# Performance work log

Measured on AMD Instinct MI355X. Metric: run time of the kernel, lower is better.

The kernel has to match this reference:

```python
import jax, jax.numpy as jnp
import numpy as np

DIM = 768
HEADS = 12
HEAD_DIM = DIM // HEADS
SCALE = HEAD_DIM ** -0.5
ALPHA = 0.1


def setup_inputs() -> dict:
    key = jax.random.key(0)
    ks = jax.random.split(key, 6)
    B, N, C = 16, 577, DIM
    x = jax.random.normal(ks[0], (B, N, C), dtype=jnp.float32)
    attn_weight = jax.random.uniform(ks[1], (B, N - 1), dtype=jnp.float32)
    w_qkv = jax.random.normal(ks[2], (C, 3 * C), dtype=jnp.float32) * (C ** -0.5)
    b_qkv = jnp.zeros((3 * C,), dtype=jnp.float32)
    w_proj = jax.random.normal(ks[3], (C, C), dtype=jnp.float32) * (C ** -0.5)
    b_proj = jnp.zeros((C,), dtype=jnp.float32)
    return {"x": x, "attn_weight": attn_weight, "w_qkv": w_qkv, "b_qkv": b_qkv,
            "w_proj": w_proj, "b_proj": b_proj}


def reference(x, attn_weight, w_qkv, b_qkv, w_proj, b_proj):
    B, N, C = x.shape
    H, D = HEADS, HEAD_DIM
    qkv = (x @ w_qkv + b_qkv).reshape(B, N, 3, H, D)
    qkv = jnp.transpose(qkv, (2, 0, 3, 1, 4))  # [3, B, H, N, D]
    q, k, v = qkv[0], qkv[1], qkv[2]
    attn = jnp.einsum('bhnd,bhmd->bhnm', q, k) * SCALE  # [B,H,N,N]
    patch_attn = attn[:, :, 0, 1:]  # pre-softmax CLS->patch scores
    # reweight CLS row (excluding CLS->CLS) before softmax
    w = attn_weight[:, None, None, :]  # [B,1,1,N-1]
    cls_row = attn[:, :, 0:1, 1:] * (w * ALPHA + (1.0 - ALPHA))
    attn = attn.at[:, :, 0:1, 1:].set(cls_row)
    attn = jax.nn.softmax(attn, axis=-1)
    out = jnp.einsum('bhnm,bhmd->bhnd', attn, v)
    out = jnp.transpose(out, (0, 2, 1, 3)).reshape(B, N, C)
    out = out @ w_proj + b_proj
    return out, patch_attn
```

## Files before the change

kernel.cpp:

```cpp
#include <hip/hip_runtime.h>
#include <hip/hip_bf16.h>
#include <math.h>

#define B_    16
#define N_    577
#define C_    768
#define H_    12
#define D_    64
#define M_    (B_ * N_)
#define MP_   9344
#define QKVN  2304
#define NP_   640
#define SCALE 0.125f
#define ALPHA 0.1f
#define OUT0  (B_ * N_ * C_)

#define NB_CONV 7008
#define NB_T1   1728
#define NB_T2   576

typedef __attribute__((ext_vector_type(8))) short short8;
typedef __attribute__((ext_vector_type(4))) float f32x4;
typedef __hip_bfloat16 bf16;

__device__ __forceinline__ float exp2fast(float x) {
    return __builtin_amdgcn_exp2f(x);
}

__device__ __forceinline__ void load16(const void* g, void* l) {
    __builtin_amdgcn_global_load_lds(
        (const __attribute__((address_space(1))) unsigned int*)g,
        (__attribute__((address_space(3))) unsigned int*)l, 16, 0, 0);
}

__device__ __forceinline__ f32x4 mfma16(short8 a, short8 b, f32x4 c) {
    return __builtin_amdgcn_mfma_f32_16x16x32_bf16(a, b, c, 0, 0, 0);
}

#define FENCE() asm volatile("" ::: "memory")
#define BARRIER() do { FENCE(); __builtin_amdgcn_s_barrier(); FENCE(); } while (0)

__global__ __launch_bounds__(256) void prep(const float* __restrict__ x,
                                            bf16* __restrict__ xb,
                                            const float* __restrict__ wq,
                                            bf16* __restrict__ wqT,
                                            const float* __restrict__ wp,
                                            bf16* __restrict__ wpT) {
    __shared__ float tile[32][33];
    const int bid = blockIdx.x;
    if (bid < NB_CONV) {
        int idx = bid * 256 + threadIdx.x;
        int m = idx / 192;
        bf16 tmp[4];
        if (m < M_) {
            float4 f = ((const float4*)x)[idx];
            tmp[0] = __float2bfloat16(f.x);
            tmp[1] = __float2bfloat16(f.y);
            tmp[2] = __float2bfloat16(f.z);
            tmp[3] = __float2bfloat16(f.w);
        } else {
            tmp[0] = tmp[1] = tmp[2] = tmp[3] = __float2bfloat16(0.f);
        }
        ((ushort4*)xb)[idx] = *(ushort4*)tmp;
        return;
    }
    const float* src; bf16* dst; int C, R, bx, by;
    if (bid < NB_CONV + NB_T1) {
        int r = bid - NB_CONV;
        bx = r % 72; by = r / 72; src = wq; dst = wqT; R = 768; C = QKVN;
    } else {
        int r = bid - NB_CONV - NB_T1;
        bx = r % 24; by = r / 24; src = wp; dst = wpT; R = 768; C = 768;
    }
    int cb = bx * 32, rb = by * 32;
    int tx = threadIdx.x & 31, ty = threadIdx.x >> 5;
    #pragma unroll
    for (int i = 0; i < 32; i += 8)
        tile[ty + i][tx] = src[(size_t)(rb + ty + i) * C + cb + tx];
    __syncthreads();
    #pragma unroll
    for (int i = 0; i < 32; i += 8)
        dst[(size_t)(cb + ty + i) * R + rb + tx] = __float2bfloat16(tile[tx][ty + i]);
}

__global__ __launch_bounds__(256, 4) void gemm128(const bf16* __restrict__ A,
                                                  const bf16* __restrict__ BT,
                                                  const float* __restrict__ bias,
                                                  bf16* __restrict__ q,
                                                  bf16* __restrict__ kk,
                                                  bf16* __restrict__ vt,
                                                  float* __restrict__ out,
                                                  int mode, int nby) {
    __shared__ __align__(16) char smem[35840];

    const int nwg = gridDim.x;
    const int orig = blockIdx.x;
    const int xcd = orig & 7, ii = orig >> 3;
    const int qq = nwg >> 3, rr = nwg & 7;
    const int wg = (xcd < rr ? xcd * (qq + 1) : rr * (qq + 1) + (xcd - rr) * qq) + ii;
    const int mb = wg / nby;
    const int nb = wg - mb * nby;
    const int m0 = mb * 128, n0 = nb * 128;
    const int t = threadIdx.x, lane = t & 63, w = t >> 6;
    const int wr = w >> 1, wc = w & 1;
    const int r16 = lane & 15, quad = lane >> 4;

    f32x4 acc[4][4];
    #pragma unroll
    for (int i = 0; i < 4; i++)
        #pragma unroll
        for (int j = 0; j < 4; j++) acc[i][j] = (f32x4)(0.f);

    const int lrow = lane >> 3;
    const int clog = ((lane & 7) ^ lrow) << 4;
    const char* gA = (const char*)A  + (size_t)(m0 + w * 32 + lrow) * 1536 + clog;
    const char* gB = (const char*)BT + (size_t)(n0 + w * 32 + lrow) * 1536 + clog;

    auto stage = [&](int k2) {
        const int kc = k2 * 128;
        #pragma unroll
        for (int i = 0; i < 4; i++) {
            char* dA = (char*)smem + w * 4096 + i * 1024;
            load16(gA + (size_t)i * 12288 + kc, dA);
            load16(gB + (size_t)i * 12288 + kc, dA + 16384);
        }
    };

    stage(0);
    asm volatile("s_waitcnt vmcnt(0)" ::: "memory");
    BARRIER();

    const int sw = r16 & 7;
    const int g0 = (quad ^ sw) << 4;
    const int g1 = ((quad ^ 4) ^ sw) << 4;

    #pragma unroll 1
    for (int k = 0; k < 12; k++) {
        const char* Ap = (const char*)smem + (wr * 64 + r16) * 128;
        const char* Bp = (const char*)smem + 16384 + (wc * 64 + r16) * 128;

        short8 a[4], b[4];
        #pragma unroll
        for (int mi = 0; mi < 4; mi++) a[mi] = *(const short8*)(Ap + mi * 2048 + g0);
        #pragma unroll
        for (int nj = 0; nj < 4; nj++) b[nj] = *(const short8*)(Bp + nj * 2048 + g0);
        __builtin_amdgcn_s_setprio(1);
        #pragma unroll
        for (int mi = 0; mi < 4; mi++)
            #pragma unroll
            for (int nj = 0; nj < 4; nj++)
                acc[mi][nj] = mfma16(a[mi], b[nj], acc[mi][nj]);
        __builtin_amdgcn_s_setprio(0);

        #pragma unroll
        for (int mi = 0; mi < 4; mi++) a[mi] = *(const short8*)(Ap + mi * 2048 + g1);
        #pragma unroll
        for (int nj = 0; nj < 4; nj++) b[nj] = *(const short8*)(Bp + nj * 2048 + g1);
        __builtin_amdgcn_s_setprio(1);
        #pragma unroll
        for (int mi = 0; mi < 4; mi++)
            #pragma unroll
            for (int nj = 0; nj < 4; nj++)
                acc[mi][nj] = mfma16(a[mi], b[nj], acc[mi][nj]);
        __builtin_amdgcn_s_setprio(0);

        BARRIER();
        if (k < 11) {
            stage(k + 1);
            asm volatile("s_waitcnt vmcnt(0)" ::: "memory");
            BARRIER();
        }
    }

    float bs[4];
    #pragma unroll
    for (int nj = 0; nj < 4; nj++) bs[nj] = bias[n0 + wc * 64 + nj * 16 + r16];

    if (mode == 1) {
        #pragma unroll
        for (int mi = 0; mi < 4; mi++) {
            #pragma unroll
            for (int nj = 0; nj < 4; nj++) {
                #pragma unroll
                for (int r = 0; r < 4; r++) {
                    int m = m0 + wr * 64 + mi * 16 + quad * 4 + r;
                    if (m >= M_) continue;
                    int cc = n0 + wc * 64 + nj * 16 + r16;
                    out[(size_t)m * 768 + cc] = acc[mi][nj][r] + bs[nj];
                }
            }
        }
        return;
    }

    bf16* Tt = (bf16*)smem;
    #pragma unroll
    for (int mi = 0; mi < 4; mi++) {
        #pragma unroll
        for (int nj = 0; nj < 4; nj++) {
            bf16 pk[4];
            #pragma unroll
            for (int r = 0; r < 4; r++)
                pk[r] = __float2bfloat16(acc[mi][nj][r] + bs[nj]);
            int ccl = wc * 64 + nj * 16 + r16;
            int ml4 = wr * 64 + mi * 16 + quad * 4;
            *(uint2*)&Tt[ccl * 140 + ml4] = *(const uint2*)pk;
        }
    }
    __syncthreads();

    const int part = nb / 6;
    if (part < 2) {
        int nl = t & 127, half = t >> 7;
        int m = m0 + nl;
        if (m < M_) {
            int b = m / N_, n = m - b * N_;
            int h = (nb % 6) * 2 + half;
            bf16* dst = (part == 0 ? q : kk) + ((size_t)(b * H_ + h) * N_ + n) * 64;
            #pragma unroll
            for (int d8 = 0; d8 < 8; d8++) {
                bf16 tv[8];
                #pragma unroll
                for (int dd = 0; dd < 8; dd++)
                    tv[dd] = Tt[(half * 64 + d8 * 8 + dd) * 140 + nl];
                *(uint4*)(dst + d8 * 8) = *(const uint4*)tv;
            }
        }
    } else {
        int dr = t >> 1, seg = t & 1;
        int rem = (nb % 6) * 128 + dr;
        int h = rem >> 6, d = rem & 63;
        int mb2 = m0 + seg * 64;
        int b = mb2 / N_;
        int n = mb2 - b * N_;
        const bf16* src = Tt + dr * 140 + seg * 64;
        int i = 0;
        while (i < 64 && mb2 + i < M_) {
            if (n == N_) { b++; n = 0; }
            bf16* drow = vt + ((size_t)(b * H_ + h) * 64 + d) * NP_;
            if ((n & 7) == 0 && n + 8 <= N_ && i + 8 <= 64 && mb2 + i + 8 <= M_) {
                bf16 tv[8];
                #pragma unroll
                for (int dd = 0; dd < 8; dd++) tv[dd] = src[i + dd];
                *(uint4*)(drow + n) = *(const uint4*)tv;
                i += 8; n += 8;
            } else {
                drow[n] = src[i]; i++; n++;
            }
        }
    }
}

__global__ __launch_bounds__(256) void attn_mfma(const bf16* __restrict__ q,
                                                 const bf16* __restrict__ k,
                                                 const bf16* __restrict__ vt,
                                                 const float* __restrict__ aw,
                                                 bf16* __restrict__ ao,
                                                 float* __restrict__ patch) {
    __shared__ bf16 Kb[2][4096];
    __shared__ bf16 Vb[2][4096];
    __shared__ bf16 Pb[4][2048];
    const int orig = blockIdx.x;
    const int wg = (orig & 7) * 120 + (orig >> 3);
    const int bh = wg / 5, qt = wg - bh * 5;
    const int b = bh / H_, h = bh - b * H_;
    const int t = threadIdx.x, lane = t & 63, w = t >> 6;
    const int r16 = lane & 15, quad = lane >> 4;
    const float SC2 = SCALE * 1.44269504f;

    const bf16* kbp = k + (size_t)bh * N_ * 64;
    const bf16* vbp = vt + (size_t)bh * 64 * NP_;

    short8 qa0[2], qa1[2];
    #pragma unroll
    for (int mi = 0; mi < 2; mi++) {
        int qrow = qt * 128 + w * 32 + mi * 16 + r16;
        int qrc = (qrow < N_) ? qrow : (N_ - 1);
        const bf16* qp = q + ((size_t)bh * N_ + qrc) * 64 + quad * 8;
        qa0[mi] = *(const short8*)(qp);
        qa1[mi] = *(const short8*)(qp + 32);
    }

    f32x4 Oacc[2][4];
    #pragma unroll
    for (int mi = 0; mi < 2; mi++)
        #pragma unroll
        for (int d0 = 0; d0 < 4; d0++) Oacc[mi][d0] = (f32x4)(0.f);
    float lrow[2][4];
    #pragma unroll
    for (int mi = 0; mi < 2; mi++)
        #pragma unroll
        for (int rr = 0; rr < 4; rr++) lrow[mi][rr] = 0.f;

    const bool clsrow = (qt == 0) && (w == 0) && (quad == 0);

    auto stage = [&](int kt, int buf) {
        #pragma unroll
        for (int is = 0; is < 2; is++) {
            int base = is * 256 + w * 64;
            int slot = base + lane;
            int row = slot >> 3, pos = slot & 7;
            int c = pos ^ (row & 7);
            int jg = kt * 64 + row; if (jg > N_ - 1) jg = N_ - 1;
            load16(kbp + (size_t)jg * 64 + c * 8, &Kb[buf][base * 8]);
        }
        #pragma unroll
        for (int is = 0; is < 2; is++) {
            int base = is * 256 + w * 64;
            int slot = base + lane;
            int row = slot >> 3, pos = slot & 7;
            int c = pos ^ (row & 7);
            load16(vbp + (size_t)row * NP_ + kt * 64 + c * 8, &Vb[buf][base * 8]);
        }
    };

    stage(0, 0);
    __syncthreads();

    for (int kt = 0; kt < 10; kt++) {
        const int cur = kt & 1;
        if (kt < 9) stage(kt + 1, cur ^ 1);

        f32x4 S[2][4];
        #pragma unroll
        for (int j0 = 0; j0 < 4; j0++) {
            int row = j0 * 16 + r16;
            const bf16* kpl = &Kb[cur][row * 64];
            short8 kf0 = *(const short8*)(kpl + ((quad ^ (row & 7)) << 3));
            short8 kf1 = *(const short8*)(kpl + (((quad ^ 4) ^ (row & 7)) << 3));
            #pragma unroll
            for (int mi = 0; mi < 2; mi++) {
                f32x4 sa = (f32x4)(0.f);
                sa = mfma16(qa0[mi], kf0, sa);
                sa = mfma16(qa1[mi], kf1, sa);
                S[mi][j0] = sa;
            }
        }

        if (kt < 9) {
            #pragma unroll
            for (int mi = 0; mi < 2; mi++) {
                #pragma unroll
                for (int j0 = 0; j0 < 4; j0++) {
                    float wfac = 1.f;
                    if (mi == 0 && clsrow) {
                        int c = kt * 64 + j0 * 16 + r16;
                        if (c >= 1) {
                            patch[(size_t)bh * (N_ - 1) + (c - 1)] = S[0][j0][0] * SCALE;
                            wfac = aw[b * (N_ - 1) + (c - 1)] * ALPHA + (1.f - ALPHA);
                        }
                    }
                    #pragma unroll
                    for (int rr = 0; rr < 4; rr++) {
                        float v = S[mi][j0][rr] * SC2;
                        if (rr == 0) v *= wfac;
                        float p = exp2fast(v);
                        S[mi][j0][rr] = p;
                        lrow[mi][rr] += p;
                    }
                }
            }
        } else {
            #pragma unroll
            for (int mi = 0; mi < 2; mi++) {
                #pragma unroll
                for (int j0 = 0; j0 < 4; j0++) {
                    int c = kt * 64 + j0 * 16 + r16;
                    bool valid = (c < N_);
                    float wfac = 1.f;
                    if (mi == 0 && clsrow && valid) {
                        patch[(size_t)bh * (N_ - 1) + (c - 1)] = S[0][j0][0] * SCALE;
                        wfac = aw[b * (N_ - 1) + (c - 1)] * ALPHA + (1.f - ALPHA);
                    }
                    #pragma unroll
                    for (int rr = 0; rr < 4; rr++) {
                        float v = S[mi][j0][rr] * SC2;
                        if (rr == 0) v *= wfac;
                        float p = valid ? exp2fast(v) : 0.f;
                        S[mi][j0][rr] = p;
                        lrow[mi][rr] += p;
                    }
                }
            }
        }

        bf16* pw = &Pb[w][0];
        #pragma unroll
        for (int mi = 0; mi < 2; mi++) {
            #pragma unroll
            for (int j0 = 0; j0 < 4; j0++) {
                int cg = j0 * 2 + (r16 >> 3);
                #pragma unroll
                for (int rr = 0; rr < 4; rr++) {
                    int rp = mi * 16 + quad * 4 + rr;
                    pw[rp * 64 + ((cg ^ (rp & 7)) << 3) + (r16 & 7)] =
                        __float2bfloat16(S[mi][j0][rr]);
                }
            }
        }
        short8 pa0[2], pa1[2];
        #pragma unroll
        for (int mi = 0; mi < 2; mi++) {
            int rp = mi * 16 + r16;
            const bf16* pr = pw + rp * 64;
            pa0[mi] = *(const short8*)(pr + ((quad ^ (rp & 7)) << 3));
            pa1[mi] = *(const short8*)(pr + (((quad ^ 4) ^ (rp & 7)) << 3));
        }

        #pragma unroll
        for (int d0 = 0; d0 < 4; d0++) {
            int row = d0 * 16 + r16;
            const bf16* vpl = &Vb[cur][row * 64];
            short8 vf0 = *(const short8*)(vpl + ((quad ^ (row & 7)) << 3));
            short8 vf1 = *(const short8*)(vpl + (((quad ^ 4) ^ (row & 7)) << 3));
            #pragma unroll
            for (int mi = 0; mi < 2; mi++) {
                Oacc[mi][d0] = mfma16(pa0[mi], vf0, Oacc[mi][d0]);
                Oacc[mi][d0] = mfma16(pa1[mi], vf1, Oacc[mi][d0]);
            }
        }
        __syncthreads();
    }

    #pragma unroll
    for (int mi = 0; mi < 2; mi++) {
        #pragma unroll
        for (int rr = 0; rr < 4; rr++) {
            float l = lrow[mi][rr];
            l += __shfl_xor(l, 1);
            l += __shfl_xor(l, 2);
            l += __shfl_xor(l, 4);
            l += __shfl_xor(l, 8);
            int n = qt * 128 + w * 32 + mi * 16 + quad * 4 + rr;
            if (n >= N_) continue;
            float inv = 1.f / l;
            #pragma unroll
            for (int d0 = 0; d0 < 4; d0++) {
                ao[((size_t)(b * N_ + n) * H_ + h) * 64 + d0 * 16 + r16] =
                    __float2bfloat16(Oacc[mi][d0][rr] * inv);
            }
        }
    }
}

extern "C" void kernel_launch(void* const* d_in, const int* in_sizes, int n_in,
                              void* d_out, int out_size, void* d_ws, size_t ws_size,
                              hipStream_t stream) {
    const float* x      = (const float*)d_in[0];
    const float* aw     = (const float*)d_in[1];
    const float* w_qkv  = (const float*)d_in[2];
    const float* b_qkv  = (const float*)d_in[3];
    const float* w_proj = (const float*)d_in[4];
    const float* b_proj = (const float*)d_in[5];
    float* out = (float*)d_out;

    char* ws = (char*)d_ws;
    bf16* xbf    = (bf16*)(ws);
    bf16* wqkvT  = (bf16*)(ws + 14352384);
    bf16* wprojT = (bf16*)(ws + 17891328);
    bf16* qv     = (bf16*)(ws + 19070976);
    bf16* kv     = (bf16*)(ws + 33251328);
    bf16* vt     = (bf16*)(ws + 47431680);
    bf16* ao     = xbf;

    prep<<<NB_CONV + NB_T1 + NB_T2, 256, 0, stream>>>(x, xbf, w_qkv, wqkvT, w_proj, wprojT);

    gemm128<<<73 * 18, 256, 0, stream>>>(
        xbf, wqkvT, b_qkv, qv, kv, vt, nullptr, 0, 18);

    attn_mfma<<<H_ * B_ * 5, 256, 0, stream>>>(qv, kv, vt, aw, ao, out + OUT0);

    gemm128<<<73 * 6, 256, 0, stream>>>(
        ao, wprojT, b_proj, nullptr, nullptr, nullptr, out, 1, 6);
}
```

Measured before the change: 208.5 us.

## Double-buffer A tile in LDS and load B fragments directly from global

The GEMM now double-buffers the A tile in shared memory, issuing the next stage's loads before the current MFMAs so global latency overlaps compute, and drops one barrier per k-step. B fragments are read straight from global memory into registers instead of being staged through LDS, which frees LDS and removes LDS reads for B. Launch bounds occupancy hint drops from 4 to 3 to give more registers. The risk is that uncoalesced per-lane global B loads and lower occupancy may hurt, and the B loads sit just before the MFMAs with little latency hiding.

```diff
diff --git a/kernel.cpp b/kernel.cpp
--- a/kernel.cpp
+++ b/kernel.cpp
@@ -83,7 +83,7 @@
         dst[(size_t)(cb + ty + i) * R + rb + tx] = __float2bfloat16(tile[tx][ty + i]);
 }
 
-__global__ __launch_bounds__(256, 4) void gemm128(const bf16* __restrict__ A,
+__global__ __launch_bounds__(256, 3) void gemm128(const bf16* __restrict__ A,
                                                   const bf16* __restrict__ BT,
                                                   const float* __restrict__ bias,
                                                   bf16* __restrict__ q,
@@ -113,18 +113,17 @@
 
     const int lrow = lane >> 3;
     const int clog = ((lane & 7) ^ lrow) << 4;
-    const char* gA = (const char*)A  + (size_t)(m0 + w * 32 + lrow) * 1536 + clog;
-    const char* gB = (const char*)BT + (size_t)(n0 + w * 32 + lrow) * 1536 + clog;
+    const char* gA = (const char*)A + (size_t)(m0 + w * 32 + lrow) * 1536 + clog;
 
     auto stage = [&](int k2) {
         const int kc = k2 * 128;
-        #pragma unroll
-        for (int i = 0; i < 4; i++) {
-            char* dA = (char*)smem + w * 4096 + i * 1024;
-            load16(gA + (size_t)i * 12288 + kc, dA);
-            load16(gB + (size_t)i * 12288 + kc, dA + 16384);
-        }
+        char* dA = (char*)smem + (k2 & 1) * 16384 + w * 4096;
+        #pragma unroll
+        for (int i = 0; i < 4; i++)
+            load16(gA + (size_t)i * 12288 + kc, dA + i * 1024);
     };
+
+    const bf16* pb = BT + (size_t)(n0 + wc * 64 + r16) * 768 + quad * 8;
 
     stage(0);
     asm volatile("s_waitcnt vmcnt(0)" ::: "memory");
@@ -136,40 +135,38 @@
 
     #pragma unroll 1
     for (int k = 0; k < 12; k++) {
-        const char* Ap = (const char*)smem + (wr * 64 + r16) * 128;
-        const char* Bp = (const char*)smem + 16384 + (wc * 64 + r16) * 128;
-
-        short8 a[4], b[4];
+        const char* Ap = (const char*)smem + (k & 1) * 16384 + (wr * 64 + r16) * 128;
+        short8 a[4], b0[4], b1[4];
+
+        #pragma unroll
+        for (int nj = 0; nj < 4; nj++) {
+            b0[nj] = *(const short8*)(pb + nj * 12288 + k * 64);
+            b1[nj] = *(const short8*)(pb + nj * 12288 + k * 64 + 32);
+        }
+        if (k < 11) stage(k + 1);
+
         #pragma unroll
         for (int mi = 0; mi < 4; mi++) a[mi] = *(const short8*)(Ap + mi * 2048 + g0);
-        #pragma unroll
-        for (int nj = 0; nj < 4; nj++) b[nj] = *(const short8*)(Bp + nj * 2048 + g0);
         __builtin_amdgcn_s_setprio(1);
         #pragma unroll
         for (int mi = 0; mi < 4; mi++)
             #pragma unroll
             for (int nj = 0; nj < 4; nj++)
-                acc[mi][nj] = mfma16(a[mi], b[nj], acc[mi][nj]);
+                acc[mi][nj] = mfma16(a[mi], b0[nj], acc[mi][nj]);
         __builtin_amdgcn_s_setprio(0);
 
         #pragma unroll
         for (int mi = 0; mi < 4; mi++) a[mi] = *(const short8*)(Ap + mi * 2048 + g1);
-        #pragma unroll
-        for (int nj = 0; nj < 4; nj++) b[nj] = *(const short8*)(Bp + nj * 2048 + g1);
         __builtin_amdgcn_s_setprio(1);
         #pragma unroll
         for (int mi = 0; mi < 4; mi++)
             #pragma unroll
             for (int nj = 0; nj < 4; nj++)
-                acc[mi][nj] = mfma16(a[mi], b[nj], acc[mi][nj]);
+                acc[mi][nj] = mfma16(a[mi], b1[nj], acc[mi][nj]);
         __builtin_amdgcn_s_setprio(0);
 
+        if (k < 11) { asm volatile("s_waitcnt vmcnt(0)" ::: "memory"); }
         BARRIER();
-        if (k < 11) {
-            stage(k + 1);
-            asm volatile("s_waitcnt vmcnt(0)" ::: "memory");
-            BARRIER();
-        }
     }
 
     float bs[4];
@@ -194,6 +191,7 @@
     }
 
     bf16* Tt = (bf16*)smem;
+    __syncthreads();
     #pragma unroll
     for (int mi = 0; mi < 4; mi++) {
         #pragma unroll
```

Result: slower. 261.5 us (+25.4%).

## Widen GEMM tiles to 128x256 with 512-thread workgroups

Applied to the files above, without the earlier changes.

The bf16 MFMA GEMM now computes a 128x256 output tile per workgroup using 8 waves (2x4) instead of a 128x128 tile with 4 waves. The A tile is shared across twice as many output columns, which cuts global and LDS traffic for A. The epilogue is split into two phases that reuse the same LDS transpose buffer for q/k/vt scatter. The price is fewer workgroups (657 and 219), which may underfill the GPU, plus higher LDS use per block.

```diff
diff --git a/kernel.cpp b/kernel.cpp
--- a/kernel.cpp
+++ b/kernel.cpp
@@ -83,15 +83,15 @@
         dst[(size_t)(cb + ty + i) * R + rb + tx] = __float2bfloat16(tile[tx][ty + i]);
 }
 
-__global__ __launch_bounds__(256, 4) void gemm128(const bf16* __restrict__ A,
-                                                  const bf16* __restrict__ BT,
-                                                  const float* __restrict__ bias,
-                                                  bf16* __restrict__ q,
-                                                  bf16* __restrict__ kk,
-                                                  bf16* __restrict__ vt,
-                                                  float* __restrict__ out,
-                                                  int mode, int nby) {
-    __shared__ __align__(16) char smem[35840];
+__global__ __launch_bounds__(512, 6) void gemmn(const bf16* __restrict__ A,
+                                                const bf16* __restrict__ BT,
+                                                const float* __restrict__ bias,
+                                                bf16* __restrict__ q,
+                                                bf16* __restrict__ kk,
+                                                bf16* __restrict__ vt,
+                                                float* __restrict__ out,
+                                                int mode, int nby) {
+    __shared__ __align__(16) char smem[49152];
 
     const int nwg = gridDim.x;
     const int orig = blockIdx.x;
@@ -100,9 +100,9 @@
     const int wg = (xcd < rr ? xcd * (qq + 1) : rr * (qq + 1) + (xcd - rr) * qq) + ii;
     const int mb = wg / nby;
     const int nb = wg - mb * nby;
-    const int m0 = mb * 128, n0 = nb * 128;
+    const int m0 = mb * 128, n0 = nb * 256;
     const int t = threadIdx.x, lane = t & 63, w = t >> 6;
-    const int wr = w >> 1, wc = w & 1;
+    const int wr = w >> 2, wc = w & 3;
     const int r16 = lane & 15, quad = lane >> 4;
 
     f32x4 acc[4][4];
@@ -113,16 +113,17 @@
 
     const int lrow = lane >> 3;
     const int clog = ((lane & 7) ^ lrow) << 4;
-    const char* gA = (const char*)A  + (size_t)(m0 + w * 32 + lrow) * 1536 + clog;
-    const char* gB = (const char*)BT + (size_t)(n0 + w * 32 + lrow) * 1536 + clog;
+    const char* gA = (const char*)A  + (size_t)(m0 + lrow) * 1536 + clog;
+    const char* gB = (const char*)BT + (size_t)(n0 + lrow) * 1536 + clog;
 
     auto stage = [&](int k2) {
         const int kc = k2 * 128;
         #pragma unroll
-        for (int i = 0; i < 4; i++) {
-            char* dA = (char*)smem + w * 4096 + i * 1024;
-            load16(gA + (size_t)i * 12288 + kc, dA);
-            load16(gB + (size_t)i * 12288 + kc, dA + 16384);
+        for (int i = 0; i < 6; i++) {
+            const int s = w * 6 + i;
+            const char* src = (s < 16) ? (gA + (size_t)s * 12288 + kc)
+                                       : (gB + (size_t)(s - 16) * 12288 + kc);
+            load16(src, (char*)smem + s * 1024);
         }
     };
 
@@ -195,57 +196,64 @@
 
     bf16* Tt = (bf16*)smem;
     #pragma unroll
-    for (int mi = 0; mi < 4; mi++) {
-        #pragma unroll
-        for (int nj = 0; nj < 4; nj++) {
-            bf16 pk[4];
-            #pragma unroll
-            for (int r = 0; r < 4; r++)
-                pk[r] = __float2bfloat16(acc[mi][nj][r] + bs[nj]);
-            int ccl = wc * 64 + nj * 16 + r16;
-            int ml4 = wr * 64 + mi * 16 + quad * 4;
-            *(uint2*)&Tt[ccl * 140 + ml4] = *(const uint2*)pk;
-        }
-    }
-    __syncthreads();
-
-    const int part = nb / 6;
-    if (part < 2) {
-        int nl = t & 127, half = t >> 7;
-        int m = m0 + nl;
-        if (m < M_) {
-            int b = m / N_, n = m - b * N_;
-            int h = (nb % 6) * 2 + half;
-            bf16* dst = (part == 0 ? q : kk) + ((size_t)(b * H_ + h) * N_ + n) * 64;
-            #pragma unroll
-            for (int d8 = 0; d8 < 8; d8++) {
-                bf16 tv[8];
-                #pragma unroll
-                for (int dd = 0; dd < 8; dd++)
-                    tv[dd] = Tt[(half * 64 + d8 * 8 + dd) * 140 + nl];
-                *(uint4*)(dst + d8 * 8) = *(const uint4*)tv;
-            }
-        }
-    } else {
-        int dr = t >> 1, seg = t & 1;
-        int rem = (nb % 6) * 128 + dr;
-        int h = rem >> 6, d = rem & 63;
-        int mb2 = m0 + seg * 64;
-        int b = mb2 / N_;
-        int n = mb2 - b * N_;
-        const bf16* src = Tt + dr * 140 + seg * 64;
-        int i = 0;
-        while (i < 64 && mb2 + i < M_) {
-            if (n == N_) { b++; n = 0; }
-            bf16* drow = vt + ((size_t)(b * H_ + h) * 64 + d) * NP_;
-            if ((n & 7) == 0 && n + 8 <= N_ && i + 8 <= 64 && mb2 + i + 8 <= M_) {
-                bf16 tv[8];
-                #pragma unroll
-                for (int dd = 0; dd < 8; dd++) tv[dd] = src[i + dd];
-                *(uint4*)(drow + n) = *(const uint4*)tv;
-                i += 8; n += 8;
-            } else {
-                drow[n] = src[i]; i++; n++;
+    for (int ph = 0; ph < 2; ph++) {
+        __syncthreads();
+        if ((wc >> 1) == ph) {
+            #pragma unroll
+            for (int mi = 0; mi < 4; mi++) {
+                #pragma unroll
+                for (int nj = 0; nj < 4; nj++) {
+                    bf16 pk[4];
+                    #pragma unroll
+                    for (int r = 0; r < 4; r++)
+                        pk[r] = __float2bfloat16(acc[mi][nj][r] + bs[nj]);
+                    int ccl = (wc & 1) * 64 + nj * 16 + r16;
+                    int ml4 = wr * 64 + mi * 16 + quad * 4;
+                    *(uint2*)&Tt[ccl * 140 + ml4] = *(const uint2*)pk;
+                }
+            }
+        }
+        __syncthreads();
+        const int cb2 = nb * 2 + ph;
+        const int part = cb2 / 6;
+        if (part < 2) {
+            int nl = t & 127, half = (t >> 7) & 1, dup = t >> 8;
+            int m = m0 + nl;
+            if (m < M_) {
+                int b = m / N_, n = m - b * N_;
+                int h = (cb2 % 6) * 2 + half;
+                bf16* dst = (part == 0 ? q : kk) + ((size_t)(b * H_ + h) * N_ + n) * 64;
+                #pragma unroll
+                for (int d8 = 0; d8 < 4; d8++) {
+                    int d8g = dup * 4 + d8;
+                    bf16 tv[8];
+                    #pragma unroll
+                    for (int dd = 0; dd < 8; dd++)
+                        tv[dd] = Tt[(half * 64 + d8g * 8 + dd) * 140 + nl];
+                    *(uint4*)(dst + d8g * 8) = *(const uint4*)tv;
+                }
+            }
+        } else {
+            int dr = t >> 2, seg = t & 3;
+            int rem = (cb2 % 6) * 128 + dr;
+            int h = rem >> 6, d = rem & 63;
+            int mb2 = m0 + seg * 32;
+            int b = mb2 / N_;
+            int n = mb2 - b * N_;
+            const bf16* src = Tt + dr * 140 + seg * 32;
+            int i = 0;
+            while (i < 32 && mb2 + i < M_) {
+                if (n == N_) { b++; n = 0; }
+                bf16* drow = vt + ((size_t)(b * H_ + h) * 64 + d) * NP_;
+                if ((n & 7) == 0 && n + 8 <= N_ && i + 8 <= 32 && mb2 + i + 8 <= M_) {
+                    bf16 tv[8];
+                    #pragma unroll
+                    for (int dd = 0; dd < 8; dd++) tv[dd] = src[i + dd];
+                    *(uint4*)(drow + n) = *(const uint4*)tv;
+                    i += 8; n += 8;
+                } else {
+                    drow[n] = src[i]; i++; n++;
+                }
             }
         }
     }
@@ -465,11 +473,11 @@
 
     prep<<<NB_CONV + NB_T1 + NB_T2, 256, 0, stream>>>(x, xbf, w_qkv, wqkvT, w_proj, wprojT);
 
-    gemm128<<<73 * 18, 256, 0, stream>>>(
-        xbf, wqkvT, b_qkv, qv, kv, vt, nullptr, 0, 18);
+    gemmn<<<73 * 9, 512, 0, stream>>>(
+        xbf, wqkvT, b_qkv, qv, kv, vt, nullptr, 0, 9);
 
     attn_mfma<<<H_ * B_ * 5, 256, 0, stream>>>(qv, kv, vt, aw, ao, out + OUT0);
 
-    gemm128<<<73 * 6, 256, 0, stream>>>(
-        ao, wprojT, b_proj, nullptr, nullptr, nullptr, out, 1, 6);
-}
+    gemmn<<<73 * 3, 512, 0, stream>>>(
+        ao, wprojT, b_proj, nullptr, nullptr, nullptr, out, 1, 3);
+}
```

After: 640.5 us. 207% more time.
